# Kernel tuning notes

Hardware: AMD Instinct MI355X
Metric: run time of the kernel (lower is better)

## Reference

```python
import jax, jax.numpy as jnp
import numpy as np

N = 256      # n_tokens
N_OUT = 128  # n_out
B = 128
D = 64


def setup_inputs() -> dict:
    key = jax.random.key(0)
    k1, k2 = jax.random.split(key)
    k = jax.random.normal(k1, (B, N, D), dtype=jnp.float32)
    v = jax.random.normal(k2, (B, N, D), dtype=jnp.float32)
    return {"k": k, "v": v}


def _greedy_merge(k, v, n, n_out):
    b = k.shape[0]
    r = n - n_out
    ti, tj = jnp.triu_indices(n, 1)  # row-major upper-triangle pairs, [m]
    m = ti.shape[0]
    b_rge = jnp.arange(b)

    # cosine-similarity scores on the upper triangle
    kn = k / jnp.linalg.norm(k, axis=-1, keepdims=True)
    scores = jnp.einsum('bnd,bmd->bnm', kn, kn)
    scores_tri = scores[:, ti, tj]                       # [b, m]
    sort_scores = jnp.argsort(-scores_tri, axis=-1, stable=True)  # descending
    ijs = jnp.stack([ti, tj], axis=-1)                   # [m, 2]
    sorted_ijs = ijs[sort_scores]                        # [b, m, 2]

    def body(carry, _):
        groups, group_ids, sorted_masks = carry
        # first still-valid (unsuppressed) pair per batch element
        sel = jnp.argmax(sorted_masks, axis=1)           # [b]
        ij = sorted_ijs[b_rge, sel]                      # [b, 2]
        i = group_ids[b_rge, ij[:, 0]]                   # current group of token i0
        j = group_ids[b_rge, ij[:, 1]]                   # current group of token j0
        group_i = groups[b_rge, i]                       # [b, n] bool membership
        # merge group i into group j
        groups = groups.at[b_rge, j].set(groups[b_rge, j] | group_i)
        group_ids = jnp.where(group_i, j[:, None], group_ids)
        groups = groups.at[b_rge, i].set(False)
        # suppress all intra-group-j edges
        group_j = groups[b_rge, j]                       # [b, n]
        edges_tri = jnp.take(group_j, ti, axis=1) & jnp.take(group_j, tj, axis=1)  # [b, m]
        perm = jnp.take_along_axis(edges_tri, sort_scores, axis=1)
        sorted_masks = sorted_masks & ~perm
        return (groups, group_ids, sorted_masks), None

    groups0 = jnp.tile(jnp.eye(n, dtype=bool), (b, 1, 1))
    group_ids0 = jnp.tile(jnp.arange(n, dtype=jnp.int32), (b, 1))
    masks0 = jnp.ones((b, m), dtype=bool)
    (groups, _, _), _ = jax.lax.scan(body, (groups0, group_ids0, masks0), None, length=r)

    # keep the n_out surviving (non-empty) group rows, preserving row order
    alive = groups.any(-1)                                       # [b, n]
    keep = jnp.argsort(~alive, axis=1, stable=True)[:, :n_out]   # [b, n_out]
    groups = jnp.take_along_axis(groups, keep[:, :, None], axis=1)  # [b, n_out, n]
    group_sizes = groups.sum(-1)                                 # [b, n_out] int
    out = jnp.einsum('bon,bnd->bod',
                     groups / group_sizes[..., None].astype(jnp.float32), v)
    return out, group_sizes


def reference(k, v):
    return _greedy_merge(k, v, N, N_OUT)
```

## Files before the change

### kernel.cpp

```cpp
#include <hip/hip_runtime.h>
#include <stdint.h>

#define NTOK 256
#define NOUT 128
#define DIM 64
#define NB 128
#define LCAP 384
#define NSEG 4
#define KTOT 1536
#define WCAP 1024
#define PCAPA 512
#define NMERGE 128
#define KAPPA 0.24f
#define SCREEN 0.2395f
#define NTILES84 1056
#define TILES_PER_SUB84 264

__device__ __forceinline__ unsigned mono_f32(float s) {
  unsigned u = __float_as_uint(s);
  return (u & 0x80000000u) ? ~u : (u | 0x80000000u);
}

__device__ __forceinline__ unsigned long long shflx64(unsigned long long x, int m) {
  unsigned lo = (unsigned)x, hi = (unsigned)(x >> 32);
  lo = __shfl_xor(lo, m);
  hi = __shfl_xor(hi, m);
  return ((unsigned long long)hi << 32) | lo;
}

__device__ __forceinline__ void tile84(int T, int& tio, int& tjo) {
  float tf = (65.0f - sqrtf(4225.0f - 4.0f * (float)T)) * 0.5f;
  int t = (int)tf;
  if (t < 0) t = 0;
  if (t > 31) t = 31;
  while (t < 31 && 65 * (t + 1) - (t + 1) * (t + 1) <= T) ++t;
  while (t > 0 && 65 * t - t * t > T) --t;
  tio = t;
  tjo = 2 * t + (T - (65 * t - t * t));
}

#define CEX(a, b, up)                         \
  do {                                        \
    unsigned long long _a = (a), _b = (b);    \
    bool _sw = (up) ? (_a < _b) : (_a > _b);  \
    if (_sw) { (a) = _b; (b) = _a; }          \
  } while (0)

#define KEEP(v, o, km) ((km) ? ((v) > (o) ? (v) : (o)) : ((v) < (o) ? (v) : (o)))

__device__ __forceinline__ void norm_tok(const float* __restrict__ K,
                                         float* __restrict__ knT,
                                         int b, int t) {
  const float* kp = K + ((size_t)b * NTOK + t) * DIM;
  float vals[64];
  double s0 = 0.0, s1 = 0.0;
#pragma unroll
  for (int q = 0; q < 8; ++q) {
    float4 v4 = *reinterpret_cast<const float4*>(kp + q * 4);
    vals[q * 4 + 0] = v4.x; vals[q * 4 + 1] = v4.y;
    vals[q * 4 + 2] = v4.z; vals[q * 4 + 3] = v4.w;
    s0 += (double)v4.x * v4.x + (double)v4.y * v4.y +
          (double)v4.z * v4.z + (double)v4.w * v4.w;
  }
#pragma unroll
  for (int q = 8; q < 16; ++q) {
    float4 v4 = *reinterpret_cast<const float4*>(kp + q * 4);
    vals[q * 4 + 0] = v4.x; vals[q * 4 + 1] = v4.y;
    vals[q * 4 + 2] = v4.z; vals[q * 4 + 3] = v4.w;
    s1 += (double)v4.x * v4.x + (double)v4.y * v4.y +
          (double)v4.z * v4.z + (double)v4.w * v4.w;
  }
  const double nrm = sqrt(s0 + s1);
#pragma unroll
  for (int d = 0; d < 64; ++d)
    knT[d * NTOK + t] = (float)((double)vals[d] / nrm);
}

__device__ __forceinline__ void normalize_to_knT(const float* __restrict__ K,
                                                 float* __restrict__ knT,
                                                 int b, int tid) {
  const int t = tid >> 1, h = tid & 1;
  const float* kp = K + ((size_t)b * NTOK + t) * DIM + h * 32;
  double ss = 0.0;
  float vals[32];
#pragma unroll
  for (int q = 0; q < 8; ++q) {
    float4 v4 = *reinterpret_cast<const float4*>(kp + q * 4);
    vals[q * 4 + 0] = v4.x; vals[q * 4 + 1] = v4.y;
    vals[q * 4 + 2] = v4.z; vals[q * 4 + 3] = v4.w;
    ss += (double)v4.x * v4.x + (double)v4.y * v4.y +
          (double)v4.z * v4.z + (double)v4.w * v4.w;
  }
  double other = __shfl_xor(ss, 1);
  double nrm = sqrt(ss + other);
#pragma unroll
  for (int q = 0; q < 32; ++q)
    knT[(h * 32 + q) * NTOK + t] = (float)((double)vals[q] / nrm);
}

#define SMEM_A 70672
__global__ __launch_bounds__(256) void gm_gram(const float* __restrict__ K,
                                               unsigned* __restrict__ gcnt,
                                               unsigned long long* __restrict__ gkeys) {
  extern __shared__ char smem[];
  float* knT = (float*)smem;
  unsigned* lpairs = (unsigned*)(smem + 65536);
  unsigned long long* lkeys = (unsigned long long*)(smem + 67584);
  int* lmisc = (int*)(smem + 70656);

  const int tid = threadIdx.x;
  const int b = blockIdx.x >> 2, sub = blockIdx.x & 3;

  if (tid == 0) { lmisc[0] = 0; lmisc[1] = 0; }
  norm_tok(K, knT, b, tid);
  __syncthreads();

  const int base = sub * TILES_PER_SUB84;
  for (int t = tid; t < TILES_PER_SUB84; t += 256) {
    int ti, tj;
    tile84(base + t, ti, tj);
    const int i0 = ti * 8, j0 = tj * 4;

    float acc[8][4] = {};
#pragma unroll 4
    for (int d = 0; d < 64; ++d) {
      const float* row = knT + d * NTOK;
      const float4 a0 = *reinterpret_cast<const float4*>(row + i0);
      const float4 a1 = *reinterpret_cast<const float4*>(row + i0 + 4);
      const float4 bv = *reinterpret_cast<const float4*>(row + j0);
      const float aa[8] = {a0.x, a0.y, a0.z, a0.w, a1.x, a1.y, a1.z, a1.w};
      const float bb[4] = {bv.x, bv.y, bv.z, bv.w};
#pragma unroll
      for (int r = 0; r < 8; ++r)
#pragma unroll
        for (int c = 0; c < 4; ++c)
          acc[r][c] = fmaf(aa[r], bb[c], acc[r][c]);
    }
#pragma unroll
    for (int r = 0; r < 8; ++r)
#pragma unroll
      for (int c = 0; c < 4; ++c) {
        const int i = i0 + r, j = j0 + c;
        if (i < j && acc[r][c] >= SCREEN) {
          const int idx = atomicAdd(&lmisc[0], 1);
          if (idx < PCAPA) lpairs[idx] = (unsigned)((i << 8) | j);
        }
      }
  }
  __syncthreads();

  const int npRaw = lmisc[0];
  const int np = npRaw > PCAPA ? PCAPA : npRaw;
  for (int e = tid; e < np; e += 256) {
    const unsigned p = lpairs[e];
    const int i = (int)(p >> 8), j = (int)(p & 255u);
    double s = 0.0;
    for (int d = 0; d < 64; ++d)
      s = fma((double)knT[d * NTOK + i], (double)knT[d * NTOK + j], s);
    const float sf = (float)s;
    if (sf >= KAPPA) {
      const unsigned long long key =
          ((unsigned long long)mono_f32(sf) << 16) |
          (unsigned)(65535 - ((i << 8) | j));
      const int idx = atomicAdd(&lmisc[1], 1);
      if (idx < LCAP) lkeys[idx] = key;
    }
  }
  __syncthreads();

  const int nkRaw = lmisc[1];
  if (tid == 0)
    gcnt[NSEG * b + sub] =
        (npRaw > PCAPA || nkRaw > LCAP) ? 0x7FFFFFFFu : (unsigned)nkRaw;
  const int nk = nkRaw > LCAP ? LCAP : nkRaw;
  unsigned long long* seg = gkeys + (size_t)b * KTOT + (size_t)sub * LCAP;
  for (int e = tid; e < nk; e += 256) seg[e] = lkeys[e];
}

#define SMEM_W 77376
__global__ __launch_bounds__(256) void gm_walk(const float* __restrict__ K,
                                               const float* __restrict__ V,
                                               float* __restrict__ OUT,
                                               const unsigned* __restrict__ gcnt,
                                               const unsigned long long* __restrict__ gkeys) {
  extern __shared__ char smem[];
  float* knT = (float*)smem;
  float* accO = (float*)smem;
  unsigned long long* keys = (unsigned long long*)(smem + 65536);
  int* gid = (int*)(smem + 73728);
  int* cnt256 = (int*)(smem + 74752);
  int* scn = (int*)(smem + 75776);
  int* rep = (int*)(smem + 76800);
  int* misc = (int*)(smem + 77312);
  unsigned long long* red = (unsigned long long*)(smem + 77328);
  unsigned long long* bkey = (unsigned long long*)(smem + 77360);

  const int tid = threadIdx.x;
  const int lane = tid & 63;
  const int wid = tid >> 6;
  const int b = blockIdx.x;

  const unsigned m0 = gcnt[NSEG * b + 0], m1 = gcnt[NSEG * b + 1],
                 m2 = gcnt[NSEG * b + 2], m3 = gcnt[NSEG * b + 3];
  const bool segOVF = (m0 > LCAP) || (m1 > LCAP) || (m2 > LCAP) || (m3 > LCAP);
  const int n0 = m0 > LCAP ? LCAP : (int)m0;
  const int n1 = m1 > LCAP ? LCAP : (int)m1;
  const int n2 = m2 > LCAP ? LCAP : (int)m2;
  const int n3 = m3 > LCAP ? LCAP : (int)m3;
  const int off1 = n0, off2 = n0 + n1, off3 = n0 + n1 + n2;
  const int cntC = off3 + n3;
  const bool fast = !segOVF && (cntC <= WCAP);

  if (tid == 0) misc[3] = fast ? NMERGE : 0;
  gid[tid] = tid;

  {
    const unsigned long long* gk = gkeys + (size_t)b * KTOT;
    for (int dst = tid; dst < WCAP; dst += 256) {
      unsigned long long v = 0ULL;
      if (fast && dst < cntC) {
        const int seg = (dst >= off1) + (dst >= off2) + (dst >= off3);
        const int base = (seg == 0) ? 0 : (seg == 1) ? off1 : (seg == 2) ? off2 : off3;
        v = gk[seg * LCAP + (dst - base)];
      }
      keys[dst] = v;
    }
  }
  __syncthreads();

  {
    const int e0 = 4 * tid;
    unsigned long long v0 = keys[e0], v1 = keys[e0 + 1],
                       v2 = keys[e0 + 2], v3 = keys[e0 + 3];
    for (int kk = 2; kk <= WCAP; kk <<= 1) {
      for (int jj = kk >> 1; jj > 0; jj >>= 1) {
        if (jj >= 256) {
          __syncthreads();
          keys[e0] = v0; keys[e0 + 1] = v1; keys[e0 + 2] = v2; keys[e0 + 3] = v3;
          __syncthreads();
          const int p0 = e0 ^ jj;
          unsigned long long o0 = keys[p0], o1 = keys[p0 + 1],
                             o2 = keys[p0 + 2], o3 = keys[p0 + 3];
          const bool km = ((e0 & kk) == 0) == ((e0 & jj) == 0);
          v0 = KEEP(v0, o0, km); v1 = KEEP(v1, o1, km);
          v2 = KEEP(v2, o2, km); v3 = KEEP(v3, o3, km);
        } else if (jj >= 4) {
          const int m = jj >> 2;
          unsigned long long o0 = shflx64(v0, m), o1 = shflx64(v1, m),
                             o2 = shflx64(v2, m), o3 = shflx64(v3, m);
          const bool km = ((e0 & kk) == 0) == ((e0 & jj) == 0);
          v0 = KEEP(v0, o0, km); v1 = KEEP(v1, o1, km);
          v2 = KEEP(v2, o2, km); v3 = KEEP(v3, o3, km);
        } else if (jj == 2) {
          const bool up = ((e0 & kk) == 0);
          CEX(v0, v2, up); CEX(v1, v3, up);
        } else {
          bool up0, up1;
          if (kk == 2) { up0 = true; up1 = false; }
          else { up0 = up1 = ((e0 & kk) == 0); }
          CEX(v0, v1, up0); CEX(v2, v3, up1);
        }
      }
    }
    __syncthreads();
    keys[e0] = v0; keys[e0 + 1] = v1; keys[e0 + 2] = v2; keys[e0 + 3] = v3;
  }
  __syncthreads();

  if (fast && wid == 0) {
    int rg0 = lane, rg1 = 64 + lane, rg2 = 128 + lane, rg3 = 192 + lane;
    int done = 0;
    for (int cursor = 0; cursor < cntC && done < NMERGE; cursor += 64) {
      const int idx = cursor + lane;
      const unsigned long long key = (idx < cntC) ? keys[idx] : 0ULL;
      const int pi = 255 - (int)((key >> 8) & 255);
      const int pj = 255 - (int)(key & 255);
      const int sli = pi & 63, ssi = pi >> 6;
      const int slj = pj & 63, ssj = pj >> 6;
      const int a0 = __shfl(rg0, sli), a1 = __shfl(rg1, sli),
                a2 = __shfl(rg2, sli), a3 = __shfl(rg3, sli);
      const int b0 = __shfl(rg0, slj), b1 = __shfl(rg1, slj),
                b2 = __shfl(rg2, slj), b3 = __shfl(rg3, slj);
      int gpi = (ssi == 0) ? a0 : (ssi == 1) ? a1 : (ssi == 2) ? a2 : a3;
      int gpj = (ssj == 0) ? b0 : (ssj == 1) ? b1 : (ssj == 2) ? b2 : b3;
      if (key == 0ULL) { gpi = 0; gpj = 0; }
      for (;;) {
        const unsigned long long mask = __ballot(gpi != gpj);
        if (!mask) break;
        const int f = __ffsll((long long)mask) - 1;
        const int gi = __shfl(gpi, f), gj = __shfl(gpj, f);
        if (lane == f) gpi = gpj;
        if (gpi == gi) gpi = gj;
        if (gpj == gi) gpj = gj;
        if (rg0 == gi) rg0 = gj;
        if (rg1 == gi) rg1 = gj;
        if (rg2 == gi) rg2 = gj;
        if (rg3 == gi) rg3 = gj;
        if (++done == NMERGE) break;
      }
    }
    gid[lane] = rg0; gid[64 + lane] = rg1;
    gid[128 + lane] = rg2; gid[192 + lane] = rg3;
    if (lane == 0) misc[3] = done;
  }
  __syncthreads();

  {
    const int start = misc[3];
    if (start < NMERGE) {
      norm_tok(K, knT, b, tid);
      __syncthreads();
      for (int mg = start; mg < NMERGE; ++mg) {
        unsigned long long best = 0ULL;
        const int p = tid >> 1, q = tid & 1;
        const int jA = 128 + p, jB = 127 - p;
        const int lenA = jA;
        const int s0 = q * 128, s1 = (q == 1) ? 255 : 128;
        for (int e = s0; e < s1; ++e) {
          const int i = (e < lenA) ? e : (e - lenA);
          const int j = (e < lenA) ? jA : jB;
          if (gid[i] != gid[j]) {
            double s = 0.0;
            for (int d = 0; d < 64; ++d)
              s = fma((double)knT[d * NTOK + i], (double)knT[d * NTOK + j], s);
            const unsigned long long key =
                ((unsigned long long)mono_f32((float)s) << 16) |
                (unsigned)(65535 - ((i << 8) | j));
            if (key > best) best = key;
          }
        }
#pragma unroll
        for (int off = 32; off; off >>= 1) {
          unsigned long long o = __shfl_down(best, off);
          if (o > best) best = o;
        }
        if (lane == 0) red[wid] = best;
        __syncthreads();
        if (tid == 0) {
          unsigned long long mx = red[0];
          for (int w = 1; w < 4; ++w)
            if (red[w] > mx) mx = red[w];
          bkey[0] = mx;
        }
        __syncthreads();
        const unsigned long long bk = bkey[0];
        const int pi = 255 - (int)((bk >> 8) & 255);
        const int pj = 255 - (int)(bk & 255);
        const int gi = gid[pi], gj = gid[pj];
        __syncthreads();
        if (gid[tid] == gi) gid[tid] = gj;
        __syncthreads();
      }
    }
  }
  __syncthreads();

  cnt256[tid] = 0;
  for (int e = tid; e < NOUT * DIM; e += 256) accO[e] = 0.0f;
  __syncthreads();
  atomicAdd(&cnt256[gid[tid]], 1);
  __syncthreads();
  if (wid == 0) {
    const int t4 = lane * 4;
    const int c0 = cnt256[t4 + 0] != 0, c1 = cnt256[t4 + 1] != 0,
              c2 = cnt256[t4 + 2] != 0, c3 = cnt256[t4 + 3] != 0;
    const int tot = c0 + c1 + c2 + c3;
    int run = tot;
#pragma unroll
    for (int off = 1; off < 64; off <<= 1) {
      int o = __shfl_up(run, off);
      if (lane >= off) run += o;
    }
    const int bs = run - tot;
    scn[t4 + 0] = bs + c0;
    scn[t4 + 1] = bs + c0 + c1;
    scn[t4 + 2] = bs + c0 + c1 + c2;
    scn[t4 + 3] = bs + tot;
  }
  __syncthreads();
  if (cnt256[tid]) rep[scn[tid] - 1] = tid;
  __syncthreads();

  {
    const int slot = scn[gid[tid]] - 1;
    const float* vp = V + ((size_t)b * NTOK + tid) * DIM;
    float* dst = accO + slot * DIM;
#pragma unroll
    for (int q = 0; q < 16; ++q) {
      float4 v4 = *reinterpret_cast<const float4*>(vp + q * 4);
      atomicAdd(&dst[q * 4 + 0], v4.x);
      atomicAdd(&dst[q * 4 + 1], v4.y);
      atomicAdd(&dst[q * 4 + 2], v4.z);
      atomicAdd(&dst[q * 4 + 3], v4.w);
    }
  }
  __syncthreads();

  float* outMain = OUT + (size_t)b * (NOUT * DIM);
  for (int e = tid; e < NOUT * DIM; e += 256) {
    const int o = e >> 6;
    const float sz = (float)cnt256[rep[o]];
    outMain[e] = accO[e] / sz;
  }
  float* outSz = OUT + (size_t)NB * NOUT * DIM + (size_t)b * NOUT;
  if (tid < NOUT) outSz[tid] = (float)cnt256[rep[tid]];
}

#define FPCAP 1024
#define FCAP 1024
#define SMEM_F 83584
__global__ __launch_bounds__(512) void gm_fused(const float* __restrict__ K,
                                                const float* __restrict__ V,
                                                float* __restrict__ OUT) {
  extern __shared__ char smem[];
  float* knT = (float*)smem;
  float* accO = (float*)smem;
  unsigned long long* keys = (unsigned long long*)(smem + 65536);
  unsigned* lpairs = (unsigned*)(smem + 73728);
  int* gid = (int*)(smem + 77824);
  int* cnt256 = (int*)(smem + 80896);
  int* scn = (int*)(smem + 81920);
  int* rep = (int*)(smem + 82944);
  unsigned long long* red = (unsigned long long*)(smem + 83456);
  unsigned long long* bkey = (unsigned long long*)(smem + 83520);
  int* misc = (int*)(smem + 83528);

  const int tid = threadIdx.x;
  const int lane = tid & 63;
  const int wid = tid >> 6;
  const int b = blockIdx.x;

  if (tid == 0) { misc[0] = 0; misc[1] = 0; }
  if (tid < NTOK) gid[tid] = tid;

  normalize_to_knT(K, knT, b, tid);
  __syncthreads();

  for (int t = tid; t < NTILES84; t += 512) {
    int ti, tj;
    tile84(t, ti, tj);
    const int i0 = ti * 8, j0 = tj * 4;
    float acc[8][4] = {};
#pragma unroll 4
    for (int d = 0; d < 64; ++d) {
      const float* row = knT + d * NTOK;
      const float4 a0 = *reinterpret_cast<const float4*>(row + i0);
      const float4 a1 = *reinterpret_cast<const float4*>(row + i0 + 4);
      const float4 bv = *reinterpret_cast<const float4*>(row + j0);
      const float aa[8] = {a0.x, a0.y, a0.z, a0.w, a1.x, a1.y, a1.z, a1.w};
      const float bb[4] = {bv.x, bv.y, bv.z, bv.w};
#pragma unroll
      for (int r = 0; r < 8; ++r)
#pragma unroll
        for (int c = 0; c < 4; ++c)
          acc[r][c] = fmaf(aa[r], bb[c], acc[r][c]);
    }
#pragma unroll
    for (int r = 0; r < 8; ++r)
#pragma unroll
      for (int c = 0; c < 4; ++c) {
        const int i = i0 + r, j = j0 + c;
        if (i < j && acc[r][c] >= SCREEN) {
          const int idx = atomicAdd(&misc[0], 1);
          if (idx < FPCAP) lpairs[idx] = (unsigned)((i << 8) | j);
        }
      }
  }
  __syncthreads();

  const int npRaw = misc[0];
  const int np = npRaw > FPCAP ? FPCAP : npRaw;
  const bool fullFB = (npRaw > FPCAP);
  for (int e = tid; e < np; e += 512) {
    const unsigned p = lpairs[e];
    const int i = (int)(p >> 8), j = (int)(p & 255u);
    double s = 0.0;
    for (int d = 0; d < 64; ++d)
      s = fma((double)knT[d * NTOK + i], (double)knT[d * NTOK + j], s);
    const float sf = (float)s;
    if (sf >= KAPPA) {
      const unsigned long long key =
          ((unsigned long long)mono_f32(sf) << 16) |
          (unsigned)(65535 - ((i << 8) | j));
      const int idx = atomicAdd(&misc[1], 1);
      keys[idx] = key;
    }
  }
  if (tid == 0) misc[3] = fullFB ? 0 : NMERGE;
  __syncthreads();
  const int nk = misc[1];

  {
    const int e0 = 2 * tid;
    unsigned long long v0 = (e0 + 0 < nk) ? keys[e0 + 0] : 0ULL;
    unsigned long long v1 = (e0 + 1 < nk) ? keys[e0 + 1] : 0ULL;
    for (int kk = 2; kk <= FCAP; kk <<= 1) {
      for (int jj = kk >> 1; jj > 0; jj >>= 1) {
        if (jj >= 128) {
          __syncthreads();
          keys[e0] = v0; keys[e0 + 1] = v1;
          __syncthreads();
          const int p0 = e0 ^ jj;
          const unsigned long long o0 = keys[p0], o1 = keys[p0 + 1];
          const bool km = ((e0 & kk) == 0) == ((e0 & jj) == 0);
          v0 = KEEP(v0, o0, km); v1 = KEEP(v1, o1, km);
        } else if (jj >= 2) {
          const int m = jj >> 1;
          const unsigned long long o0 = shflx64(v0, m), o1 = shflx64(v1, m);
          const bool km = ((e0 & kk) == 0) == ((e0 & jj) == 0);
          v0 = KEEP(v0, o0, km); v1 = KEEP(v1, o1, km);
        } else {
          const bool up = ((e0 & kk) == 0);
          CEX(v0, v1, up);
        }
      }
    }
    __syncthreads();
    keys[e0] = v0; keys[e0 + 1] = v1;
  }
  __syncthreads();

  if (misc[3] == NMERGE && wid == 0) {
    int rg0 = lane, rg1 = 64 + lane, rg2 = 128 + lane, rg3 = 192 + lane;
    int done = 0;
    for (int cursor = 0; cursor < nk && done < NMERGE; cursor += 64) {
      const int idx = cursor + lane;
      const unsigned long long key = (idx < nk) ? keys[idx] : 0ULL;
      const int pi = 255 - (int)((key >> 8) & 255);
      const int pj = 255 - (int)(key & 255);
      const int sli = pi & 63, ssi = pi >> 6;
      const int slj = pj & 63, ssj = pj >> 6;
      const int a0 = __shfl(rg0, sli), a1 = __shfl(rg1, sli),
                a2 = __shfl(rg2, sli), a3 = __shfl(rg3, sli);
      const int b0 = __shfl(rg0, slj), b1 = __shfl(rg1, slj),
                b2 = __shfl(rg2, slj), b3 = __shfl(rg3, slj);
      int gpi = (ssi == 0) ? a0 : (ssi == 1) ? a1 : (ssi == 2) ? a2 : a3;
      int gpj = (ssj == 0) ? b0 : (ssj == 1) ? b1 : (ssj == 2) ? b2 : b3;
      if (key == 0ULL) { gpi = 0; gpj = 0; }
      for (;;) {
        const unsigned long long mask = __ballot(gpi != gpj);
        if (!mask) break;
        const int f = __ffsll((long long)mask) - 1;
        const int gi = __shfl(gpi, f), gj = __shfl(gpj, f);
        if (lane == f) gpi = gpj;
        if (gpi == gi) gpi = gj;
        if (gpj == gi) gpj = gj;
        if (rg0 == gi) rg0 = gj;
        if (rg1 == gi) rg1 = gj;
        if (rg2 == gi) rg2 = gj;
        if (rg3 == gi) rg3 = gj;
        if (++done == NMERGE) break;
      }
    }
    gid[lane] = rg0; gid[64 + lane] = rg1;
    gid[128 + lane] = rg2; gid[192 + lane] = rg3;
    if (lane == 0) misc[3] = done;
  }
  __syncthreads();

  {
    const int start = misc[3];
    for (int mg = start; mg < NMERGE; ++mg) {
      unsigned long long best = 0ULL;
      const int p = tid >> 2, q = tid & 3;
      const int jA = 128 + p, jB = 127 - p;
      const int lenA = jA;
      const int s0 = q * 64, s1 = (q == 3) ? 255 : (q * 64 + 64);
      for (int e = s0; e < s1; ++e) {
        const int i = (e < lenA) ? e : (e - lenA);
        const int j = (e < lenA) ? jA : jB;
        if (gid[i] != gid[j]) {
          double s = 0.0;
          for (int d = 0; d < 64; ++d)
            s = fma((double)knT[d * NTOK + i], (double)knT[d * NTOK + j], s);
          const unsigned long long key =
              ((unsigned long long)mono_f32((float)s) << 16) |
              (unsigned)(65535 - ((i << 8) | j));
          if (key > best) best = key;
        }
      }
#pragma unroll
      for (int off = 32; off; off >>= 1) {
        unsigned long long o = __shfl_down(best, off);
        if (o > best) best = o;
      }
      if (lane == 0) red[wid] = best;
      __syncthreads();
      if (tid == 0) {
        unsigned long long mx = red[0];
        for (int w = 1; w < 8; ++w)
          if (red[w] > mx) mx = red[w];
        bkey[0] = mx;
      }
      __syncthreads();
      const unsigned long long bk = bkey[0];
      const int pi = 255 - (int)((bk >> 8) & 255);
      const int pj = 255 - (int)(bk & 255);
      const int gi = gid[pi], gj = gid[pj];
      __syncthreads();
      if (tid < NTOK && gid[tid] == gi) gid[tid] = gj;
      __syncthreads();
    }
  }
  __syncthreads();

  if (tid < NTOK) cnt256[tid] = 0;
  for (int e = tid; e < NOUT * DIM; e += 512) accO[e] = 0.0f;
  __syncthreads();
  if (tid < NTOK) atomicAdd(&cnt256[gid[tid]], 1);
  __syncthreads();
  if (wid == 0) {
    const int t4 = lane * 4;
    const int c0 = cnt256[t4 + 0] != 0, c1 = cnt256[t4 + 1] != 0,
              c2 = cnt256[t4 + 2] != 0, c3 = cnt256[t4 + 3] != 0;
    const int tot = c0 + c1 + c2 + c3;
    int run = tot;
#pragma unroll
    for (int off = 1; off < 64; off <<= 1) {
      int o = __shfl_up(run, off);
      if (lane >= off) run += o;
    }
    const int bs = run - tot;
    scn[t4 + 0] = bs + c0;
    scn[t4 + 1] = bs + c0 + c1;
    scn[t4 + 2] = bs + c0 + c1 + c2;
    scn[t4 + 3] = bs + tot;
  }
  __syncthreads();
  if (tid < NTOK && cnt256[tid]) rep[scn[tid] - 1] = tid;
  __syncthreads();

  {
    const int t = tid >> 1, h = tid & 1;
    const int slot = scn[gid[t]] - 1;
    const float* vp = V + ((size_t)b * NTOK + t) * DIM + h * 32;
    float* dst = accO + slot * DIM + h * 32;
#pragma unroll
    for (int q = 0; q < 8; ++q) {
      float4 v4 = *reinterpret_cast<const float4*>(vp + q * 4);
      atomicAdd(&dst[q * 4 + 0], v4.x);
      atomicAdd(&dst[q * 4 + 1], v4.y);
      atomicAdd(&dst[q * 4 + 2], v4.z);
      atomicAdd(&dst[q * 4 + 3], v4.w);
    }
  }
  __syncthreads();

  float* outMain = OUT + (size_t)b * (NOUT * DIM);
  for (int e = tid; e < NOUT * DIM; e += 512) {
    const int o = e >> 6;
    const float sz = (float)cnt256[rep[o]];
    outMain[e] = accO[e] / sz;
  }
  float* outSz = OUT + (size_t)NB * NOUT * DIM + (size_t)b * NOUT;
  for (int o = tid; o < NOUT; o += 512) outSz[o] = (float)cnt256[rep[o]];
}

extern "C" void kernel_launch(void* const* d_in, const int* in_sizes, int n_in,
                              void* d_out, int out_size, void* d_ws, size_t ws_size,
                              hipStream_t stream) {
  const float* K = (const float*)d_in[0];
  const float* V = (const float*)d_in[1];
  float* OUT = (float*)d_out;
  (void)in_sizes; (void)n_in; (void)out_size;

  const size_t need = 4096 + (size_t)NB * KTOT * sizeof(unsigned long long);
  if (ws_size >= need) {
    unsigned* gcnt = (unsigned*)d_ws;
    unsigned long long* gkeys = (unsigned long long*)((char*)d_ws + 4096);
    hipFuncSetAttribute(reinterpret_cast<const void*>(gm_gram),
                        hipFuncAttributeMaxDynamicSharedMemorySize, SMEM_A);
    hipFuncSetAttribute(reinterpret_cast<const void*>(gm_walk),
                        hipFuncAttributeMaxDynamicSharedMemorySize, SMEM_W);
    gm_gram<<<dim3(NB * 4), dim3(256), SMEM_A, stream>>>(K, gcnt, gkeys);
    gm_walk<<<dim3(NB), dim3(256), SMEM_W, stream>>>(K, V, OUT, gcnt, gkeys);
  } else {
    hipFuncSetAttribute(reinterpret_cast<const void*>(gm_fused),
                        hipFuncAttributeMaxDynamicSharedMemorySize, SMEM_F);
    gm_fused<<<dim3(NB), dim3(512), SMEM_F, stream>>>(K, V, OUT);
  }
}
```

Baseline: 85.50 us.

## Split gram into eight segments and break walk into sort, walk, epilogue kernels

The gram stage now runs eight sub-blocks per batch instead of four, each with half the tiles and a smaller key capacity. The old walk kernel is split into three launches: a separate sort kernel writes sorted keys back to the workspace, the walk kernel only computes group ids, and a new epilogue kernel does the averaging. The epilogue replaces per-element LDS float atomics with a gather where each thread pair sums the members of one group from a membership list. The aim is more gram parallelism and less atomic contention, at the cost of extra launches, global round trips for keys and group ids, and recomputing the normalized keys per gram block.

```diff
diff --git a/kernel.cpp b/kernel.cpp
--- a/kernel.cpp
+++ b/kernel.cpp
@@ -5,16 +5,16 @@
 #define NOUT 128
 #define DIM 64
 #define NB 128
-#define LCAP 384
-#define NSEG 4
-#define KTOT 1536
+#define NSEG 8
+#define LCAP 256
+#define KTOT 2048
 #define WCAP 1024
 #define PCAPA 512
 #define NMERGE 128
 #define KAPPA 0.24f
 #define SCREEN 0.2395f
 #define NTILES84 1056
-#define TILES_PER_SUB84 264
+#define TILES_PER_SUB84 132
 
 __device__ __forceinline__ unsigned mono_f32(float s) {
   unsigned u = __float_as_uint(s);
@@ -98,7 +98,7 @@
     knT[(h * 32 + q) * NTOK + t] = (float)((double)vals[q] / nrm);
 }
 
-#define SMEM_A 70672
+#define SMEM_A 69648
 __global__ __launch_bounds__(256) void gm_gram(const float* __restrict__ K,
                                                unsigned* __restrict__ gcnt,
                                                unsigned long long* __restrict__ gkeys) {
@@ -106,10 +106,10 @@
   float* knT = (float*)smem;
   unsigned* lpairs = (unsigned*)(smem + 65536);
   unsigned long long* lkeys = (unsigned long long*)(smem + 67584);
-  int* lmisc = (int*)(smem + 70656);
+  int* lmisc = (int*)(smem + 69632);
 
   const int tid = threadIdx.x;
-  const int b = blockIdx.x >> 2, sub = blockIdx.x & 3;
+  const int b = blockIdx.x >> 3, sub = blockIdx.x & 7;
 
   if (tid == 0) { lmisc[0] = 0; lmisc[1] = 0; }
   norm_tok(K, knT, b, tid);
@@ -177,54 +177,44 @@
   for (int e = tid; e < nk; e += 256) seg[e] = lkeys[e];
 }
 
-#define SMEM_W 77376
-__global__ __launch_bounds__(256) void gm_walk(const float* __restrict__ K,
-                                               const float* __restrict__ V,
-                                               float* __restrict__ OUT,
-                                               const unsigned* __restrict__ gcnt,
-                                               const unsigned long long* __restrict__ gkeys) {
-  extern __shared__ char smem[];
-  float* knT = (float*)smem;
-  float* accO = (float*)smem;
-  unsigned long long* keys = (unsigned long long*)(smem + 65536);
-  int* gid = (int*)(smem + 73728);
-  int* cnt256 = (int*)(smem + 74752);
-  int* scn = (int*)(smem + 75776);
-  int* rep = (int*)(smem + 76800);
-  int* misc = (int*)(smem + 77312);
-  unsigned long long* red = (unsigned long long*)(smem + 77328);
-  unsigned long long* bkey = (unsigned long long*)(smem + 77360);
-
+__device__ __forceinline__ void seg_info(const unsigned* __restrict__ gcnt, int b,
+                                         int n[NSEG], int offs[NSEG], int& cntC,
+                                         bool& fast) {
+  bool ovf = false;
+  int run = 0;
+#pragma unroll
+  for (int s = 0; s < NSEG; ++s) {
+    const unsigned m = gcnt[NSEG * b + s];
+    if (m > LCAP) ovf = true;
+    n[s] = m > LCAP ? LCAP : (int)m;
+    offs[s] = run;
+    run += n[s];
+  }
+  cntC = run;
+  fast = !ovf && (cntC <= WCAP);
+}
+
+__global__ __launch_bounds__(256) void gm_sort(const unsigned* __restrict__ gcnt,
+                                               unsigned long long* __restrict__ gkeys) {
+  __shared__ unsigned long long keys[WCAP];
   const int tid = threadIdx.x;
-  const int lane = tid & 63;
-  const int wid = tid >> 6;
   const int b = blockIdx.x;
 
-  const unsigned m0 = gcnt[NSEG * b + 0], m1 = gcnt[NSEG * b + 1],
-                 m2 = gcnt[NSEG * b + 2], m3 = gcnt[NSEG * b + 3];
-  const bool segOVF = (m0 > LCAP) || (m1 > LCAP) || (m2 > LCAP) || (m3 > LCAP);
-  const int n0 = m0 > LCAP ? LCAP : (int)m0;
-  const int n1 = m1 > LCAP ? LCAP : (int)m1;
-  const int n2 = m2 > LCAP ? LCAP : (int)m2;
-  const int n3 = m3 > LCAP ? LCAP : (int)m3;
-  const int off1 = n0, off2 = n0 + n1, off3 = n0 + n1 + n2;
-  const int cntC = off3 + n3;
-  const bool fast = !segOVF && (cntC <= WCAP);
-
-  if (tid == 0) misc[3] = fast ? NMERGE : 0;
-  gid[tid] = tid;
-
-  {
-    const unsigned long long* gk = gkeys + (size_t)b * KTOT;
-    for (int dst = tid; dst < WCAP; dst += 256) {
-      unsigned long long v = 0ULL;
-      if (fast && dst < cntC) {
-        const int seg = (dst >= off1) + (dst >= off2) + (dst >= off3);
-        const int base = (seg == 0) ? 0 : (seg == 1) ? off1 : (seg == 2) ? off2 : off3;
-        v = gk[seg * LCAP + (dst - base)];
-      }
-      keys[dst] = v;
-    }
+  int n[NSEG], offs[NSEG], cntC;
+  bool fast;
+  seg_info(gcnt, b, n, offs, cntC, fast);
+
+  unsigned long long* gk = gkeys + (size_t)b * KTOT;
+  for (int dst = tid; dst < WCAP; dst += 256) {
+    unsigned long long v = 0ULL;
+    if (fast && dst < cntC) {
+      int seg = 0, base = 0;
+#pragma unroll
+      for (int s = 1; s < NSEG; ++s)
+        if (dst >= offs[s]) { seg = s; base = offs[s]; }
+      v = gk[seg * LCAP + (dst - base)];
+    }
+    keys[dst] = v;
   }
   __syncthreads();
 
@@ -262,8 +252,38 @@
         }
       }
     }
-    __syncthreads();
-    keys[e0] = v0; keys[e0 + 1] = v1; keys[e0 + 2] = v2; keys[e0 + 3] = v3;
+    gk[e0] = v0; gk[e0 + 1] = v1; gk[e0 + 2] = v2; gk[e0 + 3] = v3;
+  }
+}
+
+#define SMEM_K 74816
+__global__ __launch_bounds__(256) void gm_walk(const float* __restrict__ K,
+                                               const unsigned* __restrict__ gcnt,
+                                               const unsigned long long* __restrict__ gkeys,
+                                               int* __restrict__ gidg) {
+  extern __shared__ char smem[];
+  float* knT = (float*)smem;
+  unsigned long long* keys = (unsigned long long*)(smem + 65536);
+  int* gid = (int*)(smem + 73728);
+  int* misc = (int*)(smem + 74752);
+  unsigned long long* red = (unsigned long long*)(smem + 74768);
+  unsigned long long* bkey = (unsigned long long*)(smem + 74800);
+
+  const int tid = threadIdx.x;
+  const int lane = tid & 63;
+  const int wid = tid >> 6;
+  const int b = blockIdx.x;
+
+  int n[NSEG], offs[NSEG], cntC;
+  bool fast;
+  seg_info(gcnt, b, n, offs, cntC, fast);
+
+  if (tid == 0) misc[3] = fast ? NMERGE : 0;
+  gid[tid] = tid;
+  {
+    const unsigned long long* gk = gkeys + (size_t)b * KTOT;
+#pragma unroll
+    for (int r = 0; r < 4; ++r) keys[4 * tid + r] = gk[4 * tid + r];
   }
   __syncthreads();
 
@@ -288,8 +308,8 @@
         const unsigned long long mask = __ballot(gpi != gpj);
         if (!mask) break;
         const int f = __ffsll((long long)mask) - 1;
-        const int gi = __shfl(gpi, f), gj = __shfl(gpj, f);
-        if (lane == f) gpi = gpj;
+        const int gij = __shfl((gpi << 8) | gpj, f);
+        const int gi = gij >> 8, gj = gij & 255;
         if (gpi == gi) gpi = gj;
         if (gpj == gi) gpj = gj;
         if (rg0 == gi) rg0 = gj;
@@ -354,12 +374,32 @@
     }
   }
   __syncthreads();
-
+  gidg[b * NTOK + tid] = gid[tid];
+}
+
+__global__ __launch_bounds__(256) void gm_epi(const float* __restrict__ V,
+                                              float* __restrict__ OUT,
+                                              const int* __restrict__ gidg) {
+  __shared__ int gid[NTOK];
+  __shared__ int cnt256[NTOK];
+  __shared__ int scn[NTOK];
+  __shared__ int rep[NOUT];
+  __shared__ int wcnt[NTOK];
+  __shared__ int slotStart[NOUT];
+  __shared__ int mem[NTOK];
+
+  const int tid = threadIdx.x;
+  const int lane = tid & 63;
+  const int wid = tid >> 6;
+  const int b = blockIdx.x;
+
+  gid[tid] = gidg[b * NTOK + tid];
   cnt256[tid] = 0;
-  for (int e = tid; e < NOUT * DIM; e += 256) accO[e] = 0.0f;
+  wcnt[tid] = 0;
   __syncthreads();
   atomicAdd(&cnt256[gid[tid]], 1);
   __syncthreads();
+
   if (wid == 0) {
     const int t4 = lane * 4;
     const int c0 = cnt256[t4 + 0] != 0, c1 = cnt256[t4 + 1] != 0,
@@ -381,26 +421,55 @@
   if (cnt256[tid]) rep[scn[tid] - 1] = tid;
   __syncthreads();
 
+  if (wid == 0) {
+    const int s0 = cnt256[rep[2 * lane]];
+    const int s1 = cnt256[rep[2 * lane + 1]];
+    const int pair = s0 + s1;
+    int run = pair;
+#pragma unroll
+    for (int off = 1; off < 64; off <<= 1) {
+      int o = __shfl_up(run, off);
+      if (lane >= off) run += o;
+    }
+    const int base = run - pair;
+    slotStart[2 * lane] = base;
+    slotStart[2 * lane + 1] = base + s0;
+  }
+  __syncthreads();
+
   {
-    const int slot = scn[gid[tid]] - 1;
-    const float* vp = V + ((size_t)b * NTOK + tid) * DIM;
-    float* dst = accO + slot * DIM;
-#pragma unroll
-    for (int q = 0; q < 16; ++q) {
-      float4 v4 = *reinterpret_cast<const float4*>(vp + q * 4);
-      atomicAdd(&dst[q * 4 + 0], v4.x);
-      atomicAdd(&dst[q * 4 + 1], v4.y);
-      atomicAdd(&dst[q * 4 + 2], v4.z);
-      atomicAdd(&dst[q * 4 + 3], v4.w);
-    }
-  }
-  __syncthreads();
-
-  float* outMain = OUT + (size_t)b * (NOUT * DIM);
-  for (int e = tid; e < NOUT * DIM; e += 256) {
-    const int o = e >> 6;
-    const float sz = (float)cnt256[rep[o]];
-    outMain[e] = accO[e] / sz;
+    const int g = gid[tid];
+    const int pos = atomicAdd(&wcnt[g], 1);
+    mem[slotStart[scn[g] - 1] + pos] = tid;
+  }
+  __syncthreads();
+
+  {
+    const int o = tid >> 1, h = tid & 1;
+    const int g = rep[o];
+    const int sz = cnt256[g];
+    const int st = slotStart[o];
+    float4 acc[8];
+#pragma unroll
+    for (int q = 0; q < 8; ++q) acc[q] = make_float4(0.f, 0.f, 0.f, 0.f);
+    for (int m = 0; m < sz; ++m) {
+      const int tok = mem[st + m];
+      const float* vp = V + ((size_t)b * NTOK + tok) * DIM + h * 32;
+#pragma unroll
+      for (int q = 0; q < 8; ++q) {
+        const float4 v4 = *reinterpret_cast<const float4*>(vp + q * 4);
+        acc[q].x += v4.x; acc[q].y += v4.y; acc[q].z += v4.z; acc[q].w += v4.w;
+      }
+    }
+    const float inv = 1.0f / (float)sz;
+    float* op = OUT + (size_t)b * (NOUT * DIM) + (size_t)o * DIM + h * 32;
+#pragma unroll
+    for (int q = 0; q < 8; ++q) {
+      float4 r;
+      r.x = acc[q].x * inv; r.y = acc[q].y * inv;
+      r.z = acc[q].z * inv; r.w = acc[q].w * inv;
+      *reinterpret_cast<float4*>(op + q * 4) = r;
+    }
   }
   float* outSz = OUT + (size_t)NB * NOUT * DIM + (size_t)b * NOUT;
   if (tid < NOUT) outSz[tid] = (float)cnt256[rep[tid]];
@@ -664,16 +733,20 @@
   float* OUT = (float*)d_out;
   (void)in_sizes; (void)n_in; (void)out_size;
 
-  const size_t need = 4096 + (size_t)NB * KTOT * sizeof(unsigned long long);
+  const size_t keysBytes = (size_t)NB * KTOT * sizeof(unsigned long long);
+  const size_t need = 4096 + keysBytes + (size_t)NB * NTOK * sizeof(int);
   if (ws_size >= need) {
     unsigned* gcnt = (unsigned*)d_ws;
     unsigned long long* gkeys = (unsigned long long*)((char*)d_ws + 4096);
+    int* gidg = (int*)((char*)d_ws + 4096 + keysBytes);
     hipFuncSetAttribute(reinterpret_cast<const void*>(gm_gram),
                         hipFuncAttributeMaxDynamicSharedMemorySize, SMEM_A);
     hipFuncSetAttribute(reinterpret_cast<const void*>(gm_walk),
-                        hipFuncAttributeMaxDynamicSharedMemorySize, SMEM_W);
-    gm_gram<<<dim3(NB * 4), dim3(256), SMEM_A, stream>>>(K, gcnt, gkeys);
-    gm_walk<<<dim3(NB), dim3(256), SMEM_W, stream>>>(K, V, OUT, gcnt, gkeys);
+                        hipFuncAttributeMaxDynamicSharedMemorySize, SMEM_K);
+    gm_gram<<<dim3(NB * 8), dim3(256), SMEM_A, stream>>>(K, gcnt, gkeys);
+    gm_sort<<<dim3(NB), dim3(256), 0, stream>>>(gcnt, gkeys);
+    gm_walk<<<dim3(NB), dim3(256), SMEM_K, stream>>>(K, gcnt, gkeys, gidg);
+    gm_epi<<<dim3(NB), dim3(256), 0, stream>>>(V, OUT, gidg);
   } else {
     hipFuncSetAttribute(reinterpret_cast<const void*>(gm_fused),
                         hipFuncAttributeMaxDynamicSharedMemorySize, SMEM_F);
```

Measured after the change: 106.7 us. +24.8%, slower.

## Precompute normalized keys once in a separate kernel and share via workspace

Applied to the files above, without the earlier changes.

Adds a gm_norm kernel that computes the transposed normalized K once per batch and writes it to the workspace. The gram blocks (four per batch) and the walk fallback now copy it with float4 loads instead of each recomputing the double-precision normalization. This trades redundant compute for an extra kernel launch and a global round trip of the normalized data. The change also packs two shuffles into one in the union loop and moves the accO zeroing after the rep scan.

```diff
diff --git a/kernel.cpp b/kernel.cpp
--- a/kernel.cpp
+++ b/kernel.cpp
@@ -5,8 +5,8 @@
 #define NOUT 128
 #define DIM 64
 #define NB 128
+#define NSEG 4
 #define LCAP 384
-#define NSEG 4
 #define KTOT 1536
 #define WCAP 1024
 #define PCAPA 512
@@ -15,6 +15,7 @@
 #define SCREEN 0.2395f
 #define NTILES84 1056
 #define TILES_PER_SUB84 264
+#define KNT_ELEMS (DIM * NTOK)
 
 __device__ __forceinline__ unsigned mono_f32(float s) {
   unsigned u = __float_as_uint(s);
@@ -48,11 +49,9 @@
 
 #define KEEP(v, o, km) ((km) ? ((v) > (o) ? (v) : (o)) : ((v) < (o) ? (v) : (o)))
 
-__device__ __forceinline__ void norm_tok(const float* __restrict__ K,
-                                         float* __restrict__ knT,
-                                         int b, int t) {
-  const float* kp = K + ((size_t)b * NTOK + t) * DIM;
-  float vals[64];
+__device__ __forceinline__ void norm_vals(const float* __restrict__ kp,
+                                          float* __restrict__ vals,
+                                          double& nrm) {
   double s0 = 0.0, s1 = 0.0;
 #pragma unroll
   for (int q = 0; q < 8; ++q) {
@@ -70,10 +69,7 @@
     s1 += (double)v4.x * v4.x + (double)v4.y * v4.y +
           (double)v4.z * v4.z + (double)v4.w * v4.w;
   }
-  const double nrm = sqrt(s0 + s1);
-#pragma unroll
-  for (int d = 0; d < 64; ++d)
-    knT[d * NTOK + t] = (float)((double)vals[d] / nrm);
+  nrm = sqrt(s0 + s1);
 }
 
 __device__ __forceinline__ void normalize_to_knT(const float* __restrict__ K,
@@ -98,8 +94,22 @@
     knT[(h * 32 + q) * NTOK + t] = (float)((double)vals[q] / nrm);
 }
 
+__global__ __launch_bounds__(256) void gm_norm(const float* __restrict__ K,
+                                               float* __restrict__ knTg) {
+  const int t = threadIdx.x;
+  const int b = blockIdx.x;
+  const float* kp = K + ((size_t)b * NTOK + t) * DIM;
+  float vals[64];
+  double nrm;
+  norm_vals(kp, vals, nrm);
+  float* dst = knTg + (size_t)b * KNT_ELEMS;
+#pragma unroll
+  for (int d = 0; d < 64; ++d)
+    dst[d * NTOK + t] = (float)((double)vals[d] / nrm);
+}
+
 #define SMEM_A 70672
-__global__ __launch_bounds__(256) void gm_gram(const float* __restrict__ K,
+__global__ __launch_bounds__(256) void gm_gram(const float* __restrict__ knTg,
                                                unsigned* __restrict__ gcnt,
                                                unsigned long long* __restrict__ gkeys) {
   extern __shared__ char smem[];
@@ -112,7 +122,13 @@
   const int b = blockIdx.x >> 2, sub = blockIdx.x & 3;
 
   if (tid == 0) { lmisc[0] = 0; lmisc[1] = 0; }
-  norm_tok(K, knT, b, tid);
+  {
+    const float4* src = reinterpret_cast<const float4*>(knTg + (size_t)b * KNT_ELEMS);
+    float4* dst = reinterpret_cast<float4*>(knT);
+#pragma unroll
+    for (int e = 0; e < KNT_ELEMS / 4 / 256; ++e)
+      dst[e * 256 + tid] = src[e * 256 + tid];
+  }
   __syncthreads();
 
   const int base = sub * TILES_PER_SUB84;
@@ -177,12 +193,29 @@
   for (int e = tid; e < nk; e += 256) seg[e] = lkeys[e];
 }
 
-#define SMEM_W 77376
-__global__ __launch_bounds__(256) void gm_walk(const float* __restrict__ K,
-                                               const float* __restrict__ V,
-                                               float* __restrict__ OUT,
-                                               const unsigned* __restrict__ gcnt,
-                                               const unsigned long long* __restrict__ gkeys) {
+__device__ __forceinline__ void seg_info(const unsigned* __restrict__ gcnt, int b,
+                                         int n[NSEG], int offs[NSEG], int& cntC,
+                                         bool& fast) {
+  bool ovf = false;
+  int run = 0;
+#pragma unroll
+  for (int s = 0; s < NSEG; ++s) {
+    const unsigned m = gcnt[NSEG * b + s];
+    if (m > LCAP) ovf = true;
+    n[s] = m > LCAP ? LCAP : (int)m;
+    offs[s] = run;
+    run += n[s];
+  }
+  cntC = run;
+  fast = !ovf && (cntC <= WCAP);
+}
+
+#define SMEM_S 77400
+__global__ __launch_bounds__(256) void gm_swe(const float* __restrict__ knTg,
+                                              const float* __restrict__ V,
+                                              float* __restrict__ OUT,
+                                              const unsigned* __restrict__ gcnt,
+                                              const unsigned long long* __restrict__ gkeys) {
   extern __shared__ char smem[];
   float* knT = (float*)smem;
   float* accO = (float*)smem;
@@ -193,23 +226,16 @@
   int* rep = (int*)(smem + 76800);
   int* misc = (int*)(smem + 77312);
   unsigned long long* red = (unsigned long long*)(smem + 77328);
-  unsigned long long* bkey = (unsigned long long*)(smem + 77360);
+  unsigned long long* bkey = (unsigned long long*)(smem + 77392);
 
   const int tid = threadIdx.x;
   const int lane = tid & 63;
   const int wid = tid >> 6;
   const int b = blockIdx.x;
 
-  const unsigned m0 = gcnt[NSEG * b + 0], m1 = gcnt[NSEG * b + 1],
-                 m2 = gcnt[NSEG * b + 2], m3 = gcnt[NSEG * b + 3];
-  const bool segOVF = (m0 > LCAP) || (m1 > LCAP) || (m2 > LCAP) || (m3 > LCAP);
-  const int n0 = m0 > LCAP ? LCAP : (int)m0;
-  const int n1 = m1 > LCAP ? LCAP : (int)m1;
-  const int n2 = m2 > LCAP ? LCAP : (int)m2;
-  const int n3 = m3 > LCAP ? LCAP : (int)m3;
-  const int off1 = n0, off2 = n0 + n1, off3 = n0 + n1 + n2;
-  const int cntC = off3 + n3;
-  const bool fast = !segOVF && (cntC <= WCAP);
+  int n[NSEG], offs[NSEG], cntC;
+  bool fast;
+  seg_info(gcnt, b, n, offs, cntC, fast);
 
   if (tid == 0) misc[3] = fast ? NMERGE : 0;
   gid[tid] = tid;
@@ -219,8 +245,10 @@
     for (int dst = tid; dst < WCAP; dst += 256) {
       unsigned long long v = 0ULL;
       if (fast && dst < cntC) {
-        const int seg = (dst >= off1) + (dst >= off2) + (dst >= off3);
-        const int base = (seg == 0) ? 0 : (seg == 1) ? off1 : (seg == 2) ? off2 : off3;
+        int seg = 0, base = 0;
+#pragma unroll
+        for (int s = 1; s < NSEG; ++s)
+          if (dst >= offs[s]) { seg = s; base = offs[s]; }
         v = gk[seg * LCAP + (dst - base)];
       }
       keys[dst] = v;
@@ -288,8 +316,8 @@
         const unsigned long long mask = __ballot(gpi != gpj);
         if (!mask) break;
         const int f = __ffsll((long long)mask) - 1;
-        const int gi = __shfl(gpi, f), gj = __shfl(gpj, f);
-        if (lane == f) gpi = gpj;
+        const int gij = __shfl((gpi << 8) | gpj, f);
+        const int gi = gij >> 8, gj = gij & 255;
         if (gpi == gi) gpi = gj;
         if (gpj == gi) gpj = gj;
         if (rg0 == gi) rg0 = gj;
@@ -308,7 +336,13 @@
   {
     const int start = misc[3];
     if (start < NMERGE) {
-      norm_tok(K, knT, b, tid);
+      {
+        const float4* src = reinterpret_cast<const float4*>(knTg + (size_t)b * KNT_ELEMS);
+        float4* dst = reinterpret_cast<float4*>(knT);
+#pragma unroll
+        for (int e = 0; e < KNT_ELEMS / 4 / 256; ++e)
+          dst[e * 256 + tid] = src[e * 256 + tid];
+      }
       __syncthreads();
       for (int mg = start; mg < NMERGE; ++mg) {
         unsigned long long best = 0ULL;
@@ -356,7 +390,6 @@
   __syncthreads();
 
   cnt256[tid] = 0;
-  for (int e = tid; e < NOUT * DIM; e += 256) accO[e] = 0.0f;
   __syncthreads();
   atomicAdd(&cnt256[gid[tid]], 1);
   __syncthreads();
@@ -379,6 +412,8 @@
   }
   __syncthreads();
   if (cnt256[tid]) rep[scn[tid] - 1] = tid;
+  __syncthreads();
+  for (int e = tid; e < NOUT * DIM; e += 256) accO[e] = 0.0f;
   __syncthreads();
 
   {
@@ -664,16 +699,20 @@
   float* OUT = (float*)d_out;
   (void)in_sizes; (void)n_in; (void)out_size;
 
-  const size_t need = 4096 + (size_t)NB * KTOT * sizeof(unsigned long long);
+  const size_t knTBytes = (size_t)NB * KNT_ELEMS * sizeof(float);
+  const size_t keysBytes = (size_t)NB * KTOT * sizeof(unsigned long long);
+  const size_t need = 4096 + knTBytes + keysBytes;
   if (ws_size >= need) {
     unsigned* gcnt = (unsigned*)d_ws;
-    unsigned long long* gkeys = (unsigned long long*)((char*)d_ws + 4096);
+    float* knTg = (float*)((char*)d_ws + 4096);
+    unsigned long long* gkeys = (unsigned long long*)((char*)d_ws + 4096 + knTBytes);
     hipFuncSetAttribute(reinterpret_cast<const void*>(gm_gram),
                         hipFuncAttributeMaxDynamicSharedMemorySize, SMEM_A);
-    hipFuncSetAttribute(reinterpret_cast<const void*>(gm_walk),
-                        hipFuncAttributeMaxDynamicSharedMemorySize, SMEM_W);
-    gm_gram<<<dim3(NB * 4), dim3(256), SMEM_A, stream>>>(K, gcnt, gkeys);
-    gm_walk<<<dim3(NB), dim3(256), SMEM_W, stream>>>(K, V, OUT, gcnt, gkeys);
+    hipFuncSetAttribute(reinterpret_cast<const void*>(gm_swe),
+                        hipFuncAttributeMaxDynamicSharedMemorySize, SMEM_S);
+    gm_norm<<<dim3(NB), dim3(256), 0, stream>>>(K, knTg);
+    gm_gram<<<dim3(NB * 4), dim3(256), SMEM_A, stream>>>(knTg, gcnt, gkeys);
+    gm_swe<<<dim3(NB), dim3(256), SMEM_S, stream>>>(knTg, V, OUT, gcnt, gkeys);
   } else {
     hipFuncSetAttribute(reinterpret_cast<const void*>(gm_fused),
                         hipFuncAttributeMaxDynamicSharedMemorySize, SMEM_F);
```

After: 93.14 us. 1.09x slower.
